# Kernel optimization log

Measured on AMD Instinct MI355X. Metric: run time of the kernel, lower is better.

## Reference

```python
import jax, jax.numpy as jnp
import numpy as np

N, D, HEADS = 8192, 1024, 8
SCALE = float(np.sqrt(D / HEADS))  # sqrt(dim_head) = sqrt(128)


def setup_inputs() -> dict:
    key = jax.random.key(0)
    ks = jax.random.split(key, 9)
    std = 0.02
    return {
        "x": jax.random.normal(ks[0], (N, D), dtype=jnp.float32),
        "Wq": jax.random.normal(ks[1], (D, D), dtype=jnp.float32) * std,
        "bq": jax.random.normal(ks[2], (D,), dtype=jnp.float32) * std,
        "Wk": jax.random.normal(ks[3], (D, D), dtype=jnp.float32) * std,
        "bk": jax.random.normal(ks[4], (D,), dtype=jnp.float32) * std,
        "Wv": jax.random.normal(ks[5], (D, D), dtype=jnp.float32) * std,
        "bv": jax.random.normal(ks[6], (D,), dtype=jnp.float32) * std,
        "Wo": jax.random.normal(ks[7], (D, D), dtype=jnp.float32) * std,
        "bo": jax.random.normal(ks[8], (D,), dtype=jnp.float32) * std,
    }


def reference(x, Wq, bq, Wk, bk, Wv, bv, Wo, bo):
    # torch nn.Linear: y = x @ W.T + b
    q = x @ Wq.T + bq          # [N, D]
    k = x @ Wk.T + bk          # [N, D]
    v = x @ Wv.T + bv          # [N, D]
    z = q @ k.T                # [N, N]
    att = jax.nn.softmax(z / SCALE, axis=-1)  # softmax over keys (torch dim=1 for 2D)
    out = att @ v              # [N, D]
    out = out @ Wo.T + bo      # output projection
    return out + x             # residual
```

## Files before the change

kernel.cpp:

```cpp
#include <hip/hip_runtime.h>
#include <stdint.h>


#define NTOK 8192
#define DMOD 1024
static constexpr float INV_SCALE = 0.08838834764831845f;

typedef __attribute__((ext_vector_type(8))) short short8;
typedef __attribute__((ext_vector_type(4))) float f32x4;
typedef __attribute__((ext_vector_type(8))) unsigned short u16x8;
typedef __attribute__((ext_vector_type(4))) unsigned short u16x4;

__device__ __forceinline__ unsigned short f2bf(float f) {
  union { float f; uint32_t u; } x{f};
  uint32_t r = x.u + 0x7fffu + ((x.u >> 16) & 1u);
  return (unsigned short)(r >> 16);
}
__device__ __forceinline__ float bf2f(unsigned short b) {
  return __uint_as_float(((uint32_t)b) << 16);
}
__device__ __forceinline__ void async16(void* lds, const void* g) {
  __builtin_amdgcn_global_load_lds((const __attribute__((address_space(1))) void*)g,
                                   (__attribute__((address_space(3))) void*)lds, 16, 0, 0);
}

__global__ __launch_bounds__(256) void cast_f32_bf16(const float* __restrict__ in,
                                                     unsigned short* __restrict__ out, int n4) {
  int i = blockIdx.x * 256 + threadIdx.x;
  int stride = gridDim.x * 256;
  for (; i < n4; i += stride) {
    float4 v = ((const float4*)in)[i];
    u16x4 o;
    o[0] = f2bf(v.x); o[1] = f2bf(v.y); o[2] = f2bf(v.z); o[3] = f2bf(v.w);
    ((u16x4*)out)[i] = o;
  }
}

template<int BM, int BN, int WM, int WN, bool BIAS, bool TRANS, bool F32OUT, bool RES>
__global__ __launch_bounds__(WM*WN*64, 2) void gemm_pipe(
    const unsigned short* __restrict__ A, const unsigned short* __restrict__ B,
    unsigned short* __restrict__ O16, float* __restrict__ O32,
    const float* __restrict__ bias, const float* __restrict__ resid,
    int M, int N, int K, float scale)
{
  constexpr int THREADS = WM * WN * 64;
  constexpr int M_REP = BM / (WM * 16);
  constexpr int N_REP = BN / (WN * 16);
  constexpr int ABYTES = BM * 64;
  constexpr int BBYTES = BN * 64;
  constexpr int BUFB = ABYTES + BBYTES;
  constexpr int RPR = THREADS / 4;
  static_assert(BM == BN, "square tiles only");
  static_assert(BM * 64 == RPR * 64 * 2, "2 staging rounds per operand");

  __shared__ alignas(16) char lds[4 * BUFB];

  const int t = threadIdx.x;
  const int l = t & 63, w = t >> 6;
  const int wrow = (w / WN) * (M_REP * 16);
  const int wcol = (w % WN) * (N_REP * 16);

  const int nwg = gridDim.x * gridDim.y;
  const int flat = blockIdx.y * gridDim.x + blockIdx.x;
  const int q8 = nwg >> 3, r8 = nwg & 7;
  const int xcd = flat & 7, pos = flat >> 3;
  const int swz = (xcd < r8 ? xcd * (q8 + 1) : r8 * (q8 + 1) + (xcd - r8) * q8) + pos;
  const int row0 = (swz / gridDim.x) * BM;
  const int col0 = (swz % gridDim.x) * BN;

  const int sr0 = t >> 2, sr1 = (t >> 2) + RPR;
  const int c0 = ((t & 3) ^ ((sr0 >> 1) & 3)) * 8;
  const int c1 = ((t & 3) ^ ((sr1 >> 1) & 3)) * 8;
  const unsigned short* gsrc[4];
  int ldst[4];
  gsrc[0] = A + (size_t)(row0 + sr0) * K + c0;  ldst[0] = t * 16;
  gsrc[1] = A + (size_t)(row0 + sr1) * K + c1;  ldst[1] = t * 16 + RPR * 64;
  gsrc[2] = B + (size_t)(col0 + sr0) * K + c0;  ldst[2] = ABYTES + t * 16;
  gsrc[3] = B + (size_t)(col0 + sr1) * K + c1;  ldst[3] = ABYTES + t * 16 + RPR * 64;

  int offA[M_REP], offB[N_REP];
#pragma unroll
  for (int m = 0; m < M_REP; ++m) {
    int r = wrow + m * 16 + (l & 15);
    offA[m] = r * 64 + (((l >> 4) ^ ((r >> 1) & 3)) * 16);
  }
#pragma unroll
  for (int n = 0; n < N_REP; ++n) {
    int r = wcol + n * 16 + (l & 15);
    offB[n] = ABYTES + r * 64 + (((l >> 4) ^ ((r >> 1) & 3)) * 16);
  }

  f32x4 acc[M_REP][N_REP] = {};
  const int KT = K / 32;

#pragma unroll
  for (int j = 0; j < 3; ++j) {
    char* bb = lds + j * BUFB;
#pragma unroll
    for (int s = 0; s < 4; ++s) async16(bb + ldst[s], gsrc[s] + j * 32);
  }

  for (int t3 = 0; t3 < KT; ++t3) {
    asm volatile("s_waitcnt lgkmcnt(0)" ::: "memory");
    __builtin_amdgcn_s_barrier();
    asm volatile("" ::: "memory");
    if (t3 + 3 < KT) {
      char* bb = lds + ((t3 + 3) & 3) * BUFB;
#pragma unroll
      for (int s = 0; s < 4; ++s) async16(bb + ldst[s], gsrc[s] + (size_t)(t3 + 3) * 32);
      asm volatile("s_waitcnt vmcnt(12)" ::: "memory");
    } else if (t3 + 3 == KT) {
      asm volatile("s_waitcnt vmcnt(8)" ::: "memory");
    } else if (t3 + 2 == KT) {
      asm volatile("s_waitcnt vmcnt(4)" ::: "memory");
    } else {
      asm volatile("s_waitcnt vmcnt(0)" ::: "memory");
    }
    __builtin_amdgcn_s_barrier();
    asm volatile("" ::: "memory");

    const char* bb = lds + (t3 & 3) * BUFB;
    short8 af[M_REP], bf[N_REP];
#pragma unroll
    for (int m = 0; m < M_REP; ++m) af[m] = *(const short8*)(bb + offA[m]);
#pragma unroll
    for (int n = 0; n < N_REP; ++n) bf[n] = *(const short8*)(bb + offB[n]);
#pragma unroll
    for (int m = 0; m < M_REP; ++m)
#pragma unroll
      for (int n = 0; n < N_REP; ++n)
        acc[m][n] = __builtin_amdgcn_mfma_f32_16x16x32_bf16(af[m], bf[n], acc[m][n], 0, 0, 0);
  }

  const int rr = (l >> 4) * 4;
#pragma unroll
  for (int m = 0; m < M_REP; ++m) {
#pragma unroll
    for (int n = 0; n < N_REP; ++n) {
#pragma unroll
      for (int j = 0; j < 4; ++j) {
        int r = row0 + wrow + m * 16 + rr + j;
        int c = col0 + wcol + n * 16 + (l & 15);
        float v = acc[m][n][j];
        if (BIAS) v += bias[c];
        v *= scale;
        if (RES) v += resid[(size_t)r * N + c];
        if (F32OUT) O32[(size_t)r * N + c] = v;
        else if (TRANS) O16[(size_t)c * M + r] = f2bf(v);
        else O16[(size_t)r * N + c] = f2bf(v);
      }
    }
  }
}

__global__ __launch_bounds__(256) void softmax_inplace(unsigned short* __restrict__ S) {
  __shared__ float red[8];
  const int t = threadIdx.x;
  unsigned short* rp = S + (size_t)blockIdx.x * NTOK;
  float v[32];
#pragma unroll
  for (int i = 0; i < 4; ++i) {
    u16x8 u = ((const u16x8*)rp)[t + i * 256];
#pragma unroll
    for (int j = 0; j < 8; ++j) v[i * 8 + j] = bf2f(u[j]);
  }
  float m = -1e30f;
#pragma unroll
  for (int k = 0; k < 32; ++k) m = fmaxf(m, v[k]);
#pragma unroll
  for (int o = 32; o; o >>= 1) m = fmaxf(m, __shfl_xor(m, o));
  if ((t & 63) == 0) red[t >> 6] = m;
  __syncthreads();
  m = fmaxf(fmaxf(red[0], red[1]), fmaxf(red[2], red[3]));
  float s = 0.f;
#pragma unroll
  for (int k = 0; k < 32; ++k) { v[k] = __expf(v[k] - m); s += v[k]; }
#pragma unroll
  for (int o = 32; o; o >>= 1) s += __shfl_xor(s, o);
  if ((t & 63) == 0) red[4 + (t >> 6)] = s;
  __syncthreads();
  s = red[4] + red[5] + red[6] + red[7];
  float inv = 1.0f / s;
#pragma unroll
  for (int i = 0; i < 4; ++i) {
    u16x8 u;
#pragma unroll
    for (int j = 0; j < 8; ++j) u[j] = f2bf(v[i * 8 + j] * inv);
    ((u16x8*)rp)[t + i * 256] = u;
  }
}

extern "C" void kernel_launch(void* const* d_in, const int* in_sizes, int n_in,
                              void* d_out, int out_size, void* d_ws, size_t ws_size,
                              hipStream_t stream) {
  const float* x  = (const float*)d_in[0];
  const float* Wq = (const float*)d_in[1];
  const float* bq = (const float*)d_in[2];
  const float* Wk = (const float*)d_in[3];
  const float* bk = (const float*)d_in[4];
  const float* Wv = (const float*)d_in[5];
  const float* bv = (const float*)d_in[6];
  const float* Wo = (const float*)d_in[7];
  const float* bo = (const float*)d_in[8];
  float* out = (float*)d_out;

  char* p = (char*)d_ws;
  unsigned short* xb  = (unsigned short*)p; p += (size_t)NTOK * DMOD * 2;
  unsigned short* Wqb = (unsigned short*)p; p += (size_t)DMOD * DMOD * 2;
  unsigned short* Wkb = (unsigned short*)p; p += (size_t)DMOD * DMOD * 2;
  unsigned short* Wvb = (unsigned short*)p; p += (size_t)DMOD * DMOD * 2;
  unsigned short* Wob = (unsigned short*)p; p += (size_t)DMOD * DMOD * 2;
  unsigned short* Qb  = (unsigned short*)p; p += (size_t)NTOK * DMOD * 2;
  unsigned short* Kb  = (unsigned short*)p; p += (size_t)NTOK * DMOD * 2;
  unsigned short* Vt  = (unsigned short*)p; p += (size_t)DMOD * NTOK * 2;
  unsigned short* Ob  = (unsigned short*)p; p += (size_t)NTOK * DMOD * 2;
  unsigned short* S   = (unsigned short*)p; p += (size_t)NTOK * NTOK * 2;

  cast_f32_bf16<<<dim3(2048), dim3(256), 0, stream>>>(x, xb, NTOK * DMOD / 4);
  cast_f32_bf16<<<dim3(1024), dim3(256), 0, stream>>>(Wq, Wqb, DMOD * DMOD / 4);
  cast_f32_bf16<<<dim3(1024), dim3(256), 0, stream>>>(Wk, Wkb, DMOD * DMOD / 4);
  cast_f32_bf16<<<dim3(1024), dim3(256), 0, stream>>>(Wv, Wvb, DMOD * DMOD / 4);
  cast_f32_bf16<<<dim3(1024), dim3(256), 0, stream>>>(Wo, Wob, DMOD * DMOD / 4);

  dim3 b512(512), b256(256);
  dim3 gS(NTOK / 256, NTOK / 256);
  dim3 gProj(DMOD / 128, NTOK / 128);

  gemm_pipe<128,128,2,2,true,false,false,false><<<gProj, b256, 0, stream>>>(xb, Wqb, Qb, nullptr, bq, nullptr, NTOK, DMOD, DMOD, INV_SCALE);
  gemm_pipe<128,128,2,2,true,false,false,false><<<gProj, b256, 0, stream>>>(xb, Wkb, Kb, nullptr, bk, nullptr, NTOK, DMOD, DMOD, 1.0f);
  gemm_pipe<128,128,2,2,true,true,false,false><<<gProj, b256, 0, stream>>>(xb, Wvb, Vt, nullptr, bv, nullptr, NTOK, DMOD, DMOD, 1.0f);
  gemm_pipe<256,256,2,4,false,false,false,false><<<gS, b512, 0, stream>>>(Qb, Kb, S, nullptr, nullptr, nullptr, NTOK, NTOK, DMOD, 1.0f);
  softmax_inplace<<<dim3(NTOK), b256, 0, stream>>>(S);
  gemm_pipe<128,128,2,2,false,false,false,false><<<gProj, b256, 0, stream>>>(S, Vt, Ob, nullptr, nullptr, nullptr, NTOK, DMOD, NTOK, 1.0f);
  gemm_pipe<128,128,2,2,true,false,true,true><<<gProj, b256, 0, stream>>>(Ob, Wob, nullptr, out, bo, x, NTOK, DMOD, DMOD, 1.0f);
}
```

Before: 551.7 us.

## Add 4-stage phased MFMA GEMM kernel for QK^T and PV products

Adds a new GEMM kernel with a four-buffer LDS ring that prefetches three K-tiles ahead. Each K-step is split into four phases that interleave async global-to-LDS loads, fragment reads and MFMA quadrants, using explicit vmcnt waits and s_setprio. Workgroups are remapped across the eight XCDs. The kernel is used for the score GEMM and for the attention-times-V GEMM, which also moves to a larger 256x128 tile. The goal is to hide memory latency and raise MFMA utilisation in the two dominant GEMMs. The cost is more LDS per block (128KB for the 256 tile), which limits occupancy, and the manual wait counts are fragile.

```diff
diff --git a/kernel.cpp b/kernel.cpp
--- a/kernel.cpp
+++ b/kernel.cpp
@@ -22,6 +22,14 @@
 __device__ __forceinline__ void async16(void* lds, const void* g) {
   __builtin_amdgcn_global_load_lds((const __attribute__((address_space(1))) void*)g,
                                    (__attribute__((address_space(3))) void*)lds, 16, 0, 0);
+}
+template<int N> __device__ __forceinline__ void waitvm() {
+  if constexpr (N == 0) asm volatile("s_waitcnt vmcnt(0)" ::: "memory");
+  else if constexpr (N == 3) asm volatile("s_waitcnt vmcnt(3)" ::: "memory");
+  else if constexpr (N == 4) asm volatile("s_waitcnt vmcnt(4)" ::: "memory");
+  else if constexpr (N == 6) asm volatile("s_waitcnt vmcnt(6)" ::: "memory");
+  else if constexpr (N == 8) asm volatile("s_waitcnt vmcnt(8)" ::: "memory");
+  else static_assert(N == 0, "unsupported vmcnt");
 }
 
 __global__ __launch_bounds__(256) void cast_f32_bf16(const float* __restrict__ in,
@@ -33,6 +41,137 @@
     u16x4 o;
     o[0] = f2bf(v.x); o[1] = f2bf(v.y); o[2] = f2bf(v.z); o[3] = f2bf(v.w);
     ((u16x4*)out)[i] = o;
+  }
+}
+
+template<int BM, int BN, int WM, int WN, bool BIAS, bool TRANS, bool F32OUT, bool RES>
+__global__ __launch_bounds__(WM*WN*64, 2) void gemm_8ph(
+    const unsigned short* __restrict__ A, const unsigned short* __restrict__ B,
+    unsigned short* __restrict__ O16, float* __restrict__ O32,
+    const float* __restrict__ bias, const float* __restrict__ resid,
+    int M, int N, int K, float scale)
+{
+  constexpr int THREADS = WM * WN * 64;
+  constexpr int M_REP = BM / (WM * 16);
+  constexpr int N_REP = BN / (WN * 16);
+  constexpr int M2 = M_REP / 2, N2 = N_REP / 2;
+  constexpr int ABYTES = BM * 64;
+  constexpr int BBYTES = BN * 64;
+  constexpr int BUFB = ABYTES + BBYTES;
+  constexpr int LOADS = BUFB / (THREADS * 16);
+  static_assert(M_REP >= 2 && N_REP >= 2 && (M_REP % 2 == 0) && (N_REP % 2 == 0));
+  static_assert(LOADS >= 1 && LOADS <= 4);
+  static_assert(ABYTES % (THREADS * 16) == 0, "A/B staging regions align to load boundary");
+
+  __shared__ alignas(16) char lds[4 * BUFB];
+
+  const int t = threadIdx.x;
+  const int l = t & 63, w = t >> 6;
+  const int wrow = (w / WN) * (M_REP * 16);
+  const int wcol = (w % WN) * (N_REP * 16);
+
+  const int nwg = gridDim.x * gridDim.y;
+  const int flat = blockIdx.y * gridDim.x + blockIdx.x;
+  const int q8 = nwg >> 3, r8 = nwg & 7;
+  const int xcd = flat & 7, pos = flat >> 3;
+  const int swz = (xcd < r8 ? xcd * (q8 + 1) : r8 * (q8 + 1) + (xcd - r8) * q8) + pos;
+  const int row0 = (swz / gridDim.x) * BM;
+  const int col0 = (swz % gridDim.x) * BN;
+
+  const unsigned short* gsrc[LOADS];
+  int ldst[LOADS];
+#pragma unroll
+  for (int li = 0; li < LOADS; ++li) {
+    const int byte0 = li * THREADS * 16 + t * 16;
+    int r; const unsigned short* base;
+    if (byte0 < ABYTES) { r = byte0 >> 6; base = A + (size_t)(row0 + r) * K; }
+    else { r = (byte0 - ABYTES) >> 6; base = B + (size_t)(col0 + r) * K; }
+    const int slot = (byte0 >> 4) & 3;
+    gsrc[li] = base + (slot ^ ((r >> 1) & 3)) * 8;
+    ldst[li] = byte0;
+  }
+
+  int offA[M_REP], offB[N_REP];
+#pragma unroll
+  for (int m = 0; m < M_REP; ++m) {
+    int r = wrow + m * 16 + (l & 15);
+    offA[m] = r * 64 + (((l >> 4) ^ ((r >> 1) & 3)) * 16);
+  }
+#pragma unroll
+  for (int n = 0; n < N_REP; ++n) {
+    int r = wcol + n * 16 + (l & 15);
+    offB[n] = ABYTES + r * 64 + (((l >> 4) ^ ((r >> 1) & 3)) * 16);
+  }
+
+  f32x4 acc[M_REP][N_REP] = {};
+  const int KT = K / 32;
+
+#pragma unroll
+  for (int j = 0; j < 3; ++j) {
+    char* bb = lds + j * BUFB;
+#pragma unroll
+    for (int li = 0; li < LOADS; ++li) async16(bb + ldst[li], gsrc[li] + j * 32);
+  }
+  waitvm<2 * LOADS>();
+  __builtin_amdgcn_s_barrier();
+
+  for (int t3 = 0; t3 < KT; ++t3) {
+    const char* rb = lds + (t3 & 3) * BUFB;
+    char* sb = lds + ((t3 + 3) & 3) * BUFB;
+    const bool st = (t3 + 3) < KT;
+    short8 a[M_REP], b[N_REP];
+#pragma unroll
+    for (int p = 0; p < 4; ++p) {
+      if (p < LOADS && st) async16(sb + ldst[p], gsrc[p] + (size_t)(t3 + 3) * 32);
+      if (p == 0) {
+#pragma unroll
+        for (int m = 0; m < M2; ++m) a[m] = *(const short8*)(rb + offA[m]);
+#pragma unroll
+        for (int n = 0; n < N2; ++n) b[n] = *(const short8*)(rb + offB[n]);
+      } else if (p == 1) {
+#pragma unroll
+        for (int n = N2; n < N_REP; ++n) b[n] = *(const short8*)(rb + offB[n]);
+      } else if (p == 2) {
+#pragma unroll
+        for (int m = M2; m < M_REP; ++m) a[m] = *(const short8*)(rb + offA[m]);
+      }
+      __builtin_amdgcn_s_barrier();
+      __builtin_amdgcn_s_setprio(1);
+      const int mh = (p >> 1) * M2, nh = (p & 1) * N2;
+#pragma unroll
+      for (int m = 0; m < M2; ++m)
+#pragma unroll
+        for (int n = 0; n < N2; ++n)
+          acc[mh + m][nh + n] =
+              __builtin_amdgcn_mfma_f32_16x16x32_bf16(a[mh + m], b[nh + n], acc[mh + m][nh + n], 0, 0, 0);
+      __builtin_amdgcn_s_setprio(0);
+      if (p == 3) {
+        if (st) waitvm<2 * LOADS>();
+        else if (t3 + 2 < KT) waitvm<LOADS>();
+        else waitvm<0>();
+      }
+      __builtin_amdgcn_s_barrier();
+    }
+  }
+
+  const int rr = (l >> 4) * 4;
+#pragma unroll
+  for (int m = 0; m < M_REP; ++m) {
+#pragma unroll
+    for (int n = 0; n < N_REP; ++n) {
+#pragma unroll
+      for (int j = 0; j < 4; ++j) {
+        int r = row0 + wrow + m * 16 + rr + j;
+        int c = col0 + wcol + n * 16 + (l & 15);
+        float v = acc[m][n][j];
+        if (BIAS) v += bias[c];
+        v *= scale;
+        if (RES) v += resid[(size_t)r * N + c];
+        if (F32OUT) O32[(size_t)r * N + c] = v;
+        else if (TRANS) O16[(size_t)c * M + r] = f2bf(v);
+        else O16[(size_t)r * N + c] = f2bf(v);
+      }
+    }
   }
 }
 
@@ -225,12 +364,13 @@
   dim3 b512(512), b256(256);
   dim3 gS(NTOK / 256, NTOK / 256);
   dim3 gProj(DMOD / 128, NTOK / 128);
+  dim3 gPV(DMOD / 128, NTOK / 256);
 
   gemm_pipe<128,128,2,2,true,false,false,false><<<gProj, b256, 0, stream>>>(xb, Wqb, Qb, nullptr, bq, nullptr, NTOK, DMOD, DMOD, INV_SCALE);
   gemm_pipe<128,128,2,2,true,false,false,false><<<gProj, b256, 0, stream>>>(xb, Wkb, Kb, nullptr, bk, nullptr, NTOK, DMOD, DMOD, 1.0f);
   gemm_pipe<128,128,2,2,true,true,false,false><<<gProj, b256, 0, stream>>>(xb, Wvb, Vt, nullptr, bv, nullptr, NTOK, DMOD, DMOD, 1.0f);
-  gemm_pipe<256,256,2,4,false,false,false,false><<<gS, b512, 0, stream>>>(Qb, Kb, S, nullptr, nullptr, nullptr, NTOK, NTOK, DMOD, 1.0f);
+  gemm_8ph<256,256,2,4,false,false,false,false><<<gS, b512, 0, stream>>>(Qb, Kb, S, nullptr, nullptr, nullptr, NTOK, NTOK, DMOD, 1.0f);
   softmax_inplace<<<dim3(NTOK), b256, 0, stream>>>(S);
-  gemm_pipe<128,128,2,2,false,false,false,false><<<gProj, b256, 0, stream>>>(S, Vt, Ob, nullptr, nullptr, nullptr, NTOK, DMOD, NTOK, 1.0f);
+  gemm_8ph<256,128,4,2,false,false,false,false><<<gPV, b512, 0, stream>>>(S, Vt, Ob, nullptr, nullptr, nullptr, NTOK, DMOD, NTOK, 1.0f);
   gemm_pipe<128,128,2,2,true,false,true,true><<<gProj, b256, 0, stream>>>(Ob, Wob, nullptr, out, bo, x, NTOK, DMOD, DMOD, 1.0f);
 }
```

Result: no change. 558.4 us (+1.2%).
